# Optimization experiments

Measured on AMD Instinct MI355X. Metric: run time of the kernel, lower is better.

The kernel has to match this reference:

```python
import jax, jax.numpy as jnp
import numpy as np

TAU = 1.0
ALPHA = 1.0
BETA = 0.2  # note: torch module hardcodes self.beta = 0.2 regardless of the beta arg
EPS = 1e-10


def setup_inputs() -> dict:
    key = jax.random.key(0)
    k1, k2, k3 = jax.random.split(key, 3)
    N, H = 32768, 1024
    C, d, K = 8, 128, 512  # n_codebooks, code_size, K
    hidden_state = jax.random.normal(k1, (N, H), dtype=jnp.float32)
    codes = jax.random.normal(k2, (C, d, K), dtype=jnp.float32)
    u = jax.random.uniform(k3, (N, C, K), dtype=jnp.float32)
    gumbel = -jnp.log(-jnp.log(u + EPS) + EPS)  # standard Gumbel noise
    return {"hidden_state": hidden_state, "codes": codes, "gumbel": gumbel}


def reference(hidden_state, codes, gumbel):
    N, H = hidden_state.shape
    C, d, K = codes.shape
    h = hidden_state.reshape(N, C, d)  # codebook c owns columns [c*d, (c+1)*d)

    # cosine-similarity logits: (h @ code) / ||h|| / ||code||
    logits = jnp.einsum('ncd,cdk->nck', h, codes)
    feat_norms = jnp.linalg.norm(h, axis=2, keepdims=True)        # [N, C, 1]
    code_norms = jnp.linalg.norm(codes, axis=1)                   # [C, K]
    logits = logits / feat_norms / code_norms[None, :, :]

    # gumbel-softmax with hard=True (straight-through one-hot)
    y_soft = jax.nn.softmax((logits + gumbel) / TAU, axis=-1)     # [N, C, K]
    idx = jnp.argmax(y_soft, axis=-1)                             # [N, C]
    y_hard = jax.nn.one_hot(idx, K, dtype=y_soft.dtype)
    attention = y_hard + y_soft - jax.lax.stop_gradient(y_soft)

    # quantized hidden state
    nh = jnp.einsum('nck,cdk->ncd', attention, codes)             # [N, C, d]

    # VQ commitment / codebook losses (detach == stop_gradient)
    diff_commit = jax.lax.stop_gradient(nh) - h
    diff_code = nh - jax.lax.stop_gradient(h)
    loss = BETA * jnp.sum(jnp.linalg.norm(diff_commit, axis=2)) \
         + ALPHA * jnp.sum(jnp.linalg.norm(diff_code, axis=2))

    return nh.reshape(N, H), loss
```

## Files before the change

kernel.cpp:

```cpp
#include <hip/hip_runtime.h>
#include <hip/hip_bf16.h>
#include <stdint.h>

#define NROWS 32768
#define HDIM  1024
#define CNB   8
#define DCS   128
#define KCB   512
#define ROWS_PB 128

typedef short bf16x8 __attribute__((ext_vector_type(8)));
typedef float f32x4 __attribute__((ext_vector_type(4)));

__device__ __forceinline__ unsigned f2bfu(float x) {
  union { float f; unsigned u; } v; v.f = x;
  return (v.u + 0x7fffu + ((v.u >> 16) & 1u)) >> 16;
}
__device__ __forceinline__ float bfu2f(unsigned short b) {
  union { unsigned u; float f; } v; v.u = ((unsigned)b) << 16;
  return v.f;
}
__device__ __forceinline__ void gload_lds16(const void* g, void* l) {
  __builtin_amdgcn_global_load_lds(
      (const __attribute__((address_space(1))) uint32_t*)g,
      (__attribute__((address_space(3))) uint32_t*)l, 16, 0, 0);
}

__global__ __launch_bounds__(256) void prep_kernel(
    const float* __restrict__ codes, unsigned short* __restrict__ codesB,
    float* __restrict__ cn2, float* __restrict__ loss_slot) {
  const int c = blockIdx.y;
  const int k0 = blockIdx.x * 64;
  const int t = threadIdx.x;
  const int kl = t & 63;
  const int dq = t >> 6;
  const int k = k0 + kl;
  const float* src = codes + (size_t)c * DCS * KCB + k;
  float vbuf[32];
  float acc = 0.f;
#pragma unroll
  for (int i = 0; i < 32; ++i) {
    float v = src[(size_t)(dq * 32 + i) * KCB];
    vbuf[i] = v;
    acc += v * v;
  }
  __shared__ float red[256];
  red[t] = acc;
  __syncthreads();
  const float s = red[kl] + red[kl + 64] + red[kl + 128] + red[kl + 192];
  const float rn = rsqrtf(s);
  if (t < 64) cn2[c * KCB + k0 + t] = s;

  char* dstbase = (char*)codesB + (size_t)c * 131072 + (size_t)(k >> 7) * 32768 + (k & 127) * 256;
  const unsigned swzk = (unsigned)(k & 7) << 4;
#pragma unroll
  for (int g = 0; g < 4; ++g) {
    unsigned short pk[8];
#pragma unroll
    for (int j = 0; j < 8; ++j) pk[j] = (unsigned short)f2bfu(vbuf[g * 8 + j] * rn);
    unsigned d2 = (unsigned)((dq * 32 + g * 8) * 2);
    *(uint4*)(dstbase + (d2 ^ swzk)) = *(const uint4*)pk;
  }
  if (blockIdx.x == 0 && c == 0 && t == 0) *loss_slot = 0.f;
}

__global__ __launch_bounds__(512, 4) void vq_kernel(
    const float* __restrict__ hidden, const float* __restrict__ gumbel,
    const unsigned short* __restrict__ codesB, const float* __restrict__ cn2g,
    float* __restrict__ out, float* __restrict__ loss_slot) {
  const int c = blockIdx.y;
  const int nb = blockIdx.x * ROWS_PB;
  const int tid = threadIdx.x;
  const int w = tid >> 6;
  const int l = tid & 63;
  const int l15 = l & 15;
  const int l4 = l >> 4;

  __shared__ char ldsB[2 * 32768];
  __shared__ float wloss[8];

  const char* cbase = (const char*)codesB + (size_t)c * 131072;

#define STAGE(chunk) { \
    const char* _s = cbase + (size_t)(chunk) * 32768; \
    char* _d = ldsB + ((chunk) & 1) * 32768 + w * 1024; \
    gload_lds16(_s + 0 * 8192 + tid * 16, _d + 0 * 8192); \
    gload_lds16(_s + 1 * 8192 + tid * 16, _d + 1 * 8192); \
    gload_lds16(_s + 2 * 8192 + tid * 16, _d + 2 * 8192); \
    gload_lds16(_s + 3 * 8192 + tid * 16, _d + 3 * 8192); }

  const int nrow = nb + w * 16 + l15;
  const float* hp = hidden + (size_t)nrow * HDIM + c * DCS + l4 * 8;
  f32x4 hr[4][2];
#pragma unroll
  for (int s = 0; s < 4; ++s) {
    hr[s][0] = *(const f32x4*)(hp + s * 32);
    hr[s][1] = *(const f32x4*)(hp + s * 32 + 4);
  }

  STAGE(0)
  STAGE(1)

  float hn2 = 0.f;
  float hv[4][8];
#pragma unroll
  for (int s = 0; s < 4; ++s)
#pragma unroll
    for (int j = 0; j < 4; ++j) {
      hv[s][j] = hr[s][0][j]; hv[s][4 + j] = hr[s][1][j];
    }
#pragma unroll
  for (int s = 0; s < 4; ++s)
#pragma unroll
    for (int j = 0; j < 8; ++j) hn2 += hv[s][j] * hv[s][j];
  hn2 += __shfl_xor(hn2, 16);
  hn2 += __shfl_xor(hn2, 32);
  const float hnorm = sqrtf(hn2);
  const float rh = hnorm > 0.f ? 1.0f / hnorm : 0.f;
  bf16x8 afr[4];
#pragma unroll
  for (int s = 0; s < 4; ++s)
#pragma unroll
    for (int j = 0; j < 8; ++j) afr[s][j] = (short)f2bfu(hv[s][j] * rh);

  const float* gbase = gumbel + ((size_t)nrow * CNB + c) * KCB + l4 * 4;
  const unsigned swz = (unsigned)(l15 & 7) << 4;

  float bs = -3.4e38f, ba = 0.f;
  int bk = 0;

  __syncthreads();

#pragma unroll
  for (int i = 0; i < 4; ++i) {
    const int kc = i * 128;
    const char* buf = ldsB + (i & 1) * 32768;

    f32x4 garr[8];
#pragma unroll
    for (int t = 0; t < 8; ++t)
      garr[t] = *(const f32x4*)(gbase + kc + t * 16);

    f32x4 acc[8];
#pragma unroll
    for (int t = 0; t < 8; ++t) acc[t] = (f32x4){0.f, 0.f, 0.f, 0.f};
#pragma unroll
    for (int t = 0; t < 8; ++t) {
      const unsigned rowbase = (unsigned)((t * 16 + l15) * 256);
#pragma unroll
      for (int s = 0; s < 4; ++s) {
        bf16x8 bfr = *(const bf16x8*)(buf + rowbase + (((unsigned)(s * 64 + l4 * 16)) ^ swz));
        acc[t] = __builtin_amdgcn_mfma_f32_16x16x32_bf16(bfr, afr[s], acc[t], 0, 0, 0);
      }
    }

#pragma unroll
    for (int t = 0; t < 8; ++t) {
#pragma unroll
      for (int r = 0; r < 4; ++r) {
        const int kf = kc + t * 16 + l4 * 4 + r;
        float sc = acc[t][r] + garr[t][r];
        if (sc > bs) { bs = sc; bk = kf; ba = acc[t][r]; }
      }
    }

    __syncthreads();
    if (i < 2) STAGE(i + 2)
  }

#pragma unroll
  for (int m = 16; m <= 32; m <<= 1) {
    float os = __shfl_xor(bs, m);
    int ok = __shfl_xor(bk, m);
    float oa = __shfl_xor(ba, m);
    if (os > bs || (os == bs && ok < bk)) { bs = os; bk = ok; ba = oa; }
  }

  const float c2 = cn2g[c * KCB + bk];
  const float cn = sqrtf(c2);
  const float arg = c2 + hn2 - 2.f * (ba * hnorm * cn);
  float lsum = (l4 == 0) ? sqrtf(fmaxf(arg, 0.f)) : 0.f;

  const char* cb = cbase + (size_t)(bk >> 7) * 32768 + (bk & 127) * 256;
  const unsigned swzk = (unsigned)(bk & 7) << 4;
  float* op = out + (size_t)nrow * HDIM + c * DCS + l4 * 32;
#pragma unroll
  for (int j = 0; j < 4; ++j) {
    unsigned d2 = (unsigned)((l4 * 32 + j * 8) * 2);
    bf16x8 cv = *(const bf16x8*)(cb + (d2 ^ swzk));
    f32x4 o0, o1;
#pragma unroll
    for (int e = 0; e < 4; ++e) {
      o0[e] = bfu2f((unsigned short)cv[e]) * cn;
      o1[e] = bfu2f((unsigned short)cv[4 + e]) * cn;
    }
    *(f32x4*)(op + j * 8) = o0;
    *(f32x4*)(op + j * 8 + 4) = o1;
  }

#pragma unroll
  for (int m = 1; m <= 32; m <<= 1) lsum += __shfl_xor(lsum, m);
  if (l == 0) wloss[w] = lsum;
  __syncthreads();
  if (tid == 0) {
    float tot = 0.f;
#pragma unroll
    for (int i = 0; i < 8; ++i) tot += wloss[i];
    atomicAdd(loss_slot, tot * 1.2f);
  }
#undef STAGE
}

extern "C" void kernel_launch(void* const* d_in, const int* in_sizes, int n_in,
                              void* d_out, int out_size, void* d_ws, size_t ws_size,
                              hipStream_t stream) {
  const float* hidden = (const float*)d_in[0];
  const float* codes  = (const float*)d_in[1];
  const float* gumbel = (const float*)d_in[2];
  float* out = (float*)d_out;
  unsigned short* codesB = (unsigned short*)d_ws;
  float* cn2 = (float*)((char*)d_ws + (size_t)CNB * 131072);
  float* loss_slot = out + (size_t)NROWS * HDIM;

  prep_kernel<<<dim3(8, CNB), 256, 0, stream>>>(codes, codesB, cn2, loss_slot);
  vq_kernel<<<dim3(NROWS / ROWS_PB, CNB), 512, 0, stream>>>(hidden, gumbel, codesB, cn2, out, loss_slot);
}
```

Baseline: 213.7 us.

## Halve codebook chunk size to raise occupancy and drop block-level loss reduction

Shrinks the staged codebook chunk from 128 to 64 codes, halving LDS use to 32KB and allowing 8 blocks per CU via launch bounds. The K loop becomes a non-unrolled 8-iteration loop, which lowers register pressure, and the prep kernel's layout changes to match. The final loss reduction now uses per-wave atomics instead of an LDS reduction and barrier. The trade-off is more barriers per block and more atomic traffic, in exchange for more resident waves to hide gumbel and hidden-state load latency.

```diff
diff --git a/kernel.cpp b/kernel.cpp
--- a/kernel.cpp
+++ b/kernel.cpp
@@ -8,6 +8,7 @@
 #define DCS   128
 #define KCB   512
 #define ROWS_PB 128
+#define KCHUNK 64
 
 typedef short bf16x8 __attribute__((ext_vector_type(8)));
 typedef float f32x4 __attribute__((ext_vector_type(4)));
@@ -51,7 +52,7 @@
   const float rn = rsqrtf(s);
   if (t < 64) cn2[c * KCB + k0 + t] = s;
 
-  char* dstbase = (char*)codesB + (size_t)c * 131072 + (size_t)(k >> 7) * 32768 + (k & 127) * 256;
+  char* dstbase = (char*)codesB + (size_t)c * 131072 + (size_t)(k >> 6) * 16384 + (k & 63) * 256;
   const unsigned swzk = (unsigned)(k & 7) << 4;
 #pragma unroll
   for (int g = 0; g < 4; ++g) {
@@ -64,7 +65,7 @@
   if (blockIdx.x == 0 && c == 0 && t == 0) *loss_slot = 0.f;
 }
 
-__global__ __launch_bounds__(512, 4) void vq_kernel(
+__global__ __launch_bounds__(512, 8) void vq_kernel(
     const float* __restrict__ hidden, const float* __restrict__ gumbel,
     const unsigned short* __restrict__ codesB, const float* __restrict__ cn2g,
     float* __restrict__ out, float* __restrict__ loss_slot) {
@@ -76,18 +77,15 @@
   const int l15 = l & 15;
   const int l4 = l >> 4;
 
-  __shared__ char ldsB[2 * 32768];
-  __shared__ float wloss[8];
+  __shared__ char ldsB[2 * 16384];
 
   const char* cbase = (const char*)codesB + (size_t)c * 131072;
 
 #define STAGE(chunk) { \
-    const char* _s = cbase + (size_t)(chunk) * 32768; \
-    char* _d = ldsB + ((chunk) & 1) * 32768 + w * 1024; \
-    gload_lds16(_s + 0 * 8192 + tid * 16, _d + 0 * 8192); \
-    gload_lds16(_s + 1 * 8192 + tid * 16, _d + 1 * 8192); \
-    gload_lds16(_s + 2 * 8192 + tid * 16, _d + 2 * 8192); \
-    gload_lds16(_s + 3 * 8192 + tid * 16, _d + 3 * 8192); }
+    const char* _s = cbase + (size_t)(chunk) * 16384 + w * 2048 + l * 16; \
+    char* _d = ldsB + ((chunk) & 1) * 16384 + w * 2048; \
+    gload_lds16(_s, _d); \
+    gload_lds16(_s + 1024, _d + 1024); }
 
   const int nrow = nb + w * 16 + l15;
   const float* hp = hidden + (size_t)nrow * HDIM + c * DCS + l4 * 8;
@@ -102,17 +100,10 @@
   STAGE(1)
 
   float hn2 = 0.f;
-  float hv[4][8];
 #pragma unroll
   for (int s = 0; s < 4; ++s)
 #pragma unroll
-    for (int j = 0; j < 4; ++j) {
-      hv[s][j] = hr[s][0][j]; hv[s][4 + j] = hr[s][1][j];
-    }
-#pragma unroll
-  for (int s = 0; s < 4; ++s)
-#pragma unroll
-    for (int j = 0; j < 8; ++j) hn2 += hv[s][j] * hv[s][j];
+    for (int j = 0; j < 4; ++j) hn2 += hr[s][0][j] * hr[s][0][j] + hr[s][1][j] * hr[s][1][j];
   hn2 += __shfl_xor(hn2, 16);
   hn2 += __shfl_xor(hn2, 32);
   const float hnorm = sqrtf(hn2);
@@ -121,7 +112,10 @@
 #pragma unroll
   for (int s = 0; s < 4; ++s)
 #pragma unroll
-    for (int j = 0; j < 8; ++j) afr[s][j] = (short)f2bfu(hv[s][j] * rh);
+    for (int j = 0; j < 4; ++j) {
+      afr[s][j]     = (short)f2bfu(hr[s][0][j] * rh);
+      afr[s][4 + j] = (short)f2bfu(hr[s][1][j] * rh);
+    }
 
   const float* gbase = gumbel + ((size_t)nrow * CNB + c) * KCB + l4 * 4;
   const unsigned swz = (unsigned)(l15 & 7) << 4;
@@ -131,21 +125,21 @@
 
   __syncthreads();
 
-#pragma unroll
-  for (int i = 0; i < 4; ++i) {
-    const int kc = i * 128;
-    const char* buf = ldsB + (i & 1) * 32768;
-
-    f32x4 garr[8];
-#pragma unroll
-    for (int t = 0; t < 8; ++t)
+#pragma unroll 1
+  for (int i = 0; i < 8; ++i) {
+    const int kc = i * KCHUNK;
+    const char* buf = ldsB + (i & 1) * 16384;
+
+    f32x4 garr[4];
+#pragma unroll
+    for (int t = 0; t < 4; ++t)
       garr[t] = *(const f32x4*)(gbase + kc + t * 16);
 
-    f32x4 acc[8];
-#pragma unroll
-    for (int t = 0; t < 8; ++t) acc[t] = (f32x4){0.f, 0.f, 0.f, 0.f};
-#pragma unroll
-    for (int t = 0; t < 8; ++t) {
+    f32x4 acc[4];
+#pragma unroll
+    for (int t = 0; t < 4; ++t) acc[t] = (f32x4){0.f, 0.f, 0.f, 0.f};
+#pragma unroll
+    for (int t = 0; t < 4; ++t) {
       const unsigned rowbase = (unsigned)((t * 16 + l15) * 256);
 #pragma unroll
       for (int s = 0; s < 4; ++s) {
@@ -155,7 +149,7 @@
     }
 
 #pragma unroll
-    for (int t = 0; t < 8; ++t) {
+    for (int t = 0; t < 4; ++t) {
 #pragma unroll
       for (int r = 0; r < 4; ++r) {
         const int kf = kc + t * 16 + l4 * 4 + r;
@@ -165,7 +159,7 @@
     }
 
     __syncthreads();
-    if (i < 2) STAGE(i + 2)
+    if (i < 6) STAGE(i + 2)
   }
 
 #pragma unroll
@@ -181,7 +175,7 @@
   const float arg = c2 + hn2 - 2.f * (ba * hnorm * cn);
   float lsum = (l4 == 0) ? sqrtf(fmaxf(arg, 0.f)) : 0.f;
 
-  const char* cb = cbase + (size_t)(bk >> 7) * 32768 + (bk & 127) * 256;
+  const char* cb = cbase + (size_t)(bk >> 6) * 16384 + (bk & 63) * 256;
   const unsigned swzk = (unsigned)(bk & 7) << 4;
   float* op = out + (size_t)nrow * HDIM + c * DCS + l4 * 32;
 #pragma unroll
@@ -200,14 +194,7 @@
 
 #pragma unroll
   for (int m = 1; m <= 32; m <<= 1) lsum += __shfl_xor(lsum, m);
-  if (l == 0) wloss[w] = lsum;
-  __syncthreads();
-  if (tid == 0) {
-    float tot = 0.f;
-#pragma unroll
-    for (int i = 0; i < 8; ++i) tot += wloss[i];
-    atomicAdd(loss_slot, tot * 1.2f);
-  }
+  if (l == 0) atomicAdd(loss_slot, lsum * 1.2f);
 #undef STAGE
 }
 
```

After: 305.1 us. +42.7%, slower.

## Process two row tiles per wave to reuse codebook fragments across MFMAs

Applied to the files above, without the earlier changes.

Each wave now handles 32 rows (two 16-row tiles) instead of 16, so every codebook LDS fragment read feeds two MFMAs. The block covers 256 rows, which halves the number of times each block stages its codebook into LDS. Argmax now runs right after each tile's MFMAs, the final barrier is dropped, and the per-block loss reduction through shared memory is replaced by per-wave atomics. In exchange, register pressure rises, the occupancy hint drops to 2 blocks per CU, and the loss accumulator takes eight times more atomics.

```diff
diff --git a/kernel.cpp b/kernel.cpp
--- a/kernel.cpp
+++ b/kernel.cpp
@@ -7,7 +7,7 @@
 #define CNB   8
 #define DCS   128
 #define KCB   512
-#define ROWS_PB 128
+#define ROWS_PB 256
 
 typedef short bf16x8 __attribute__((ext_vector_type(8)));
 typedef float f32x4 __attribute__((ext_vector_type(4)));
@@ -64,7 +64,7 @@
   if (blockIdx.x == 0 && c == 0 && t == 0) *loss_slot = 0.f;
 }
 
-__global__ __launch_bounds__(512, 4) void vq_kernel(
+__global__ __launch_bounds__(512, 2) void vq_kernel(
     const float* __restrict__ hidden, const float* __restrict__ gumbel,
     const unsigned short* __restrict__ codesB, const float* __restrict__ cn2g,
     float* __restrict__ out, float* __restrict__ loss_slot) {
@@ -77,7 +77,6 @@
   const int l4 = l >> 4;
 
   __shared__ char ldsB[2 * 32768];
-  __shared__ float wloss[8];
 
   const char* cbase = (const char*)codesB + (size_t)c * 131072;
 
@@ -89,45 +88,55 @@
     gload_lds16(_s + 2 * 8192 + tid * 16, _d + 2 * 8192); \
     gload_lds16(_s + 3 * 8192 + tid * 16, _d + 3 * 8192); }
 
-  const int nrow = nb + w * 16 + l15;
-  const float* hp = hidden + (size_t)nrow * HDIM + c * DCS + l4 * 8;
-  f32x4 hr[4][2];
+  const int rowA = nb + w * 32 + l15;
+  const int rowB = rowA + 16;
+  const float* hpA = hidden + (size_t)rowA * HDIM + c * DCS + l4 * 8;
+  const float* hpB = hpA + (size_t)16 * HDIM;
+  f32x4 hA0[4], hA1[4], hB0[4], hB1[4];
 #pragma unroll
   for (int s = 0; s < 4; ++s) {
-    hr[s][0] = *(const f32x4*)(hp + s * 32);
-    hr[s][1] = *(const f32x4*)(hp + s * 32 + 4);
+    hA0[s] = *(const f32x4*)(hpA + s * 32);
+    hA1[s] = *(const f32x4*)(hpA + s * 32 + 4);
+    hB0[s] = *(const f32x4*)(hpB + s * 32);
+    hB1[s] = *(const f32x4*)(hpB + s * 32 + 4);
   }
 
   STAGE(0)
   STAGE(1)
 
-  float hn2 = 0.f;
-  float hv[4][8];
+  float hn2A = 0.f, hn2B = 0.f;
 #pragma unroll
   for (int s = 0; s < 4; ++s)
 #pragma unroll
     for (int j = 0; j < 4; ++j) {
-      hv[s][j] = hr[s][0][j]; hv[s][4 + j] = hr[s][1][j];
-    }
+      hn2A += hA0[s][j] * hA0[s][j] + hA1[s][j] * hA1[s][j];
+      hn2B += hB0[s][j] * hB0[s][j] + hB1[s][j] * hB1[s][j];
+    }
+  hn2A += __shfl_xor(hn2A, 16);
+  hn2A += __shfl_xor(hn2A, 32);
+  hn2B += __shfl_xor(hn2B, 16);
+  hn2B += __shfl_xor(hn2B, 32);
+  const float hnA = sqrtf(hn2A);
+  const float hnB = sqrtf(hn2B);
+  const float rhA = hnA > 0.f ? 1.0f / hnA : 0.f;
+  const float rhB = hnB > 0.f ? 1.0f / hnB : 0.f;
+  bf16x8 afrA[4], afrB[4];
 #pragma unroll
   for (int s = 0; s < 4; ++s)
 #pragma unroll
-    for (int j = 0; j < 8; ++j) hn2 += hv[s][j] * hv[s][j];
-  hn2 += __shfl_xor(hn2, 16);
-  hn2 += __shfl_xor(hn2, 32);
-  const float hnorm = sqrtf(hn2);
-  const float rh = hnorm > 0.f ? 1.0f / hnorm : 0.f;
-  bf16x8 afr[4];
-#pragma unroll
-  for (int s = 0; s < 4; ++s)
-#pragma unroll
-    for (int j = 0; j < 8; ++j) afr[s][j] = (short)f2bfu(hv[s][j] * rh);
-
-  const float* gbase = gumbel + ((size_t)nrow * CNB + c) * KCB + l4 * 4;
+    for (int j = 0; j < 4; ++j) {
+      afrA[s][j]     = (short)f2bfu(hA0[s][j] * rhA);
+      afrA[s][4 + j] = (short)f2bfu(hA1[s][j] * rhA);
+      afrB[s][j]     = (short)f2bfu(hB0[s][j] * rhB);
+      afrB[s][4 + j] = (short)f2bfu(hB1[s][j] * rhB);
+    }
+
+  const float* gbA = gumbel + ((size_t)rowA * CNB + c) * KCB + l4 * 4;
+  const float* gbB = gbA + (size_t)16 * CNB * KCB;
   const unsigned swz = (unsigned)(l15 & 7) << 4;
 
-  float bs = -3.4e38f, ba = 0.f;
-  int bk = 0;
+  float bsA = -3.4e38f, baA = 0.f, bsB = -3.4e38f, baB = 0.f;
+  int bkA = 0, bkB = 0;
 
   __syncthreads();
 
@@ -136,79 +145,77 @@
     const int kc = i * 128;
     const char* buf = ldsB + (i & 1) * 32768;
 
-    f32x4 garr[8];
-#pragma unroll
-    for (int t = 0; t < 8; ++t)
-      garr[t] = *(const f32x4*)(gbase + kc + t * 16);
-
-    f32x4 acc[8];
-#pragma unroll
-    for (int t = 0; t < 8; ++t) acc[t] = (f32x4){0.f, 0.f, 0.f, 0.f};
+    f32x4 gA[8], gB[8];
+#pragma unroll
+    for (int t = 0; t < 8; ++t) {
+      gA[t] = *(const f32x4*)(gbA + kc + t * 16);
+      gB[t] = *(const f32x4*)(gbB + kc + t * 16);
+    }
+
 #pragma unroll
     for (int t = 0; t < 8; ++t) {
       const unsigned rowbase = (unsigned)((t * 16 + l15) * 256);
+      f32x4 accA = (f32x4){0.f, 0.f, 0.f, 0.f};
+      f32x4 accB = (f32x4){0.f, 0.f, 0.f, 0.f};
 #pragma unroll
       for (int s = 0; s < 4; ++s) {
         bf16x8 bfr = *(const bf16x8*)(buf + rowbase + (((unsigned)(s * 64 + l4 * 16)) ^ swz));
-        acc[t] = __builtin_amdgcn_mfma_f32_16x16x32_bf16(bfr, afr[s], acc[t], 0, 0, 0);
+        accA = __builtin_amdgcn_mfma_f32_16x16x32_bf16(bfr, afrA[s], accA, 0, 0, 0);
+        accB = __builtin_amdgcn_mfma_f32_16x16x32_bf16(bfr, afrB[s], accB, 0, 0, 0);
       }
-    }
-
-#pragma unroll
-    for (int t = 0; t < 8; ++t) {
 #pragma unroll
       for (int r = 0; r < 4; ++r) {
         const int kf = kc + t * 16 + l4 * 4 + r;
-        float sc = acc[t][r] + garr[t][r];
-        if (sc > bs) { bs = sc; bk = kf; ba = acc[t][r]; }
+        const float scA = accA[r] + gA[t][r];
+        if (scA > bsA) { bsA = scA; bkA = kf; baA = accA[r]; }
+        const float scB = accB[r] + gB[t][r];
+        if (scB > bsB) { bsB = scB; bkB = kf; baB = accB[r]; }
       }
     }
 
-    __syncthreads();
+    if (i < 3) __syncthreads();
     if (i < 2) STAGE(i + 2)
   }
+#undef STAGE
 
 #pragma unroll
   for (int m = 16; m <= 32; m <<= 1) {
-    float os = __shfl_xor(bs, m);
-    int ok = __shfl_xor(bk, m);
-    float oa = __shfl_xor(ba, m);
-    if (os > bs || (os == bs && ok < bk)) { bs = os; bk = ok; ba = oa; }
-  }
-
-  const float c2 = cn2g[c * KCB + bk];
-  const float cn = sqrtf(c2);
-  const float arg = c2 + hn2 - 2.f * (ba * hnorm * cn);
-  float lsum = (l4 == 0) ? sqrtf(fmaxf(arg, 0.f)) : 0.f;
-
-  const char* cb = cbase + (size_t)(bk >> 7) * 32768 + (bk & 127) * 256;
-  const unsigned swzk = (unsigned)(bk & 7) << 4;
-  float* op = out + (size_t)nrow * HDIM + c * DCS + l4 * 32;
-#pragma unroll
-  for (int j = 0; j < 4; ++j) {
-    unsigned d2 = (unsigned)((l4 * 32 + j * 8) * 2);
-    bf16x8 cv = *(const bf16x8*)(cb + (d2 ^ swzk));
-    f32x4 o0, o1;
-#pragma unroll
-    for (int e = 0; e < 4; ++e) {
-      o0[e] = bfu2f((unsigned short)cv[e]) * cn;
-      o1[e] = bfu2f((unsigned short)cv[4 + e]) * cn;
-    }
-    *(f32x4*)(op + j * 8) = o0;
-    *(f32x4*)(op + j * 8 + 4) = o1;
-  }
+    float os; int ok; float oa;
+    os = __shfl_xor(bsA, m); ok = __shfl_xor(bkA, m); oa = __shfl_xor(baA, m);
+    if (os > bsA || (os == bsA && ok < bkA)) { bsA = os; bkA = ok; baA = oa; }
+    os = __shfl_xor(bsB, m); ok = __shfl_xor(bkB, m); oa = __shfl_xor(baB, m);
+    if (os > bsB || (os == bsB && ok < bkB)) { bsB = os; bkB = ok; baB = oa; }
+  }
+
+  float lsum = 0.f;
+#define EPI(BK, HN2, HN, ROW, BA) { \
+    const float c2 = cn2g[c * KCB + (BK)]; \
+    const float cn = sqrtf(c2); \
+    const float arg = c2 + (HN2) - 2.f * ((BA) * (HN) * cn); \
+    if (l4 == 0) lsum += sqrtf(fmaxf(arg, 0.f)); \
+    const char* cb = cbase + (size_t)((BK) >> 7) * 32768 + ((BK) & 127) * 256; \
+    const unsigned swzk = (unsigned)((BK) & 7) << 4; \
+    float* op = out + (size_t)(ROW) * HDIM + c * DCS + l4 * 32; \
+    _Pragma("unroll") \
+    for (int j = 0; j < 4; ++j) { \
+      unsigned d2 = (unsigned)((l4 * 32 + j * 8) * 2); \
+      bf16x8 cv = *(const bf16x8*)(cb + (d2 ^ swzk)); \
+      f32x4 o0, o1; \
+      _Pragma("unroll") \
+      for (int e = 0; e < 4; ++e) { \
+        o0[e] = bfu2f((unsigned short)cv[e]) * cn; \
+        o1[e] = bfu2f((unsigned short)cv[4 + e]) * cn; \
+      } \
+      *(f32x4*)(op + j * 8) = o0; \
+      *(f32x4*)(op + j * 8 + 4) = o1; \
+    } }
+  EPI(bkA, hn2A, hnA, rowA, baA)
+  EPI(bkB, hn2B, hnB, rowB, baB)
+#undef EPI
 
 #pragma unroll
   for (int m = 1; m <= 32; m <<= 1) lsum += __shfl_xor(lsum, m);
-  if (l == 0) wloss[w] = lsum;
-  __syncthreads();
-  if (tid == 0) {
-    float tot = 0.f;
-#pragma unroll
-    for (int i = 0; i < 8; ++i) tot += wloss[i];
-    atomicAdd(loss_slot, tot * 1.2f);
-  }
-#undef STAGE
+  if (l == 0) atomicAdd(loss_slot, lsum * 1.2f);
 }
 
 extern "C" void kernel_launch(void* const* d_in, const int* in_sizes, int n_in,
```

Result: slower. 451.2 us (+111.1%).
